# Performance work log

Measured on AMD Instinct MI355X. Metric: run time of the kernel, lower is better.

The kernel has to match this reference:

```python
import jax, jax.numpy as jnp
import numpy as np

N_EMBD = 384
N_HEAD = 6
HEAD_SIZE = N_EMBD // N_HEAD
D_FF = 4 * N_EMBD
LN_EPS = 1e-3  # keras LayerNormalization default epsilon


def setup_inputs() -> dict:
    key = jax.random.key(0)
    ks = jax.random.split(key, 12)
    B, T = 4, 2048
    s = 1.0 / np.sqrt(N_EMBD)
    return {
        "x": jax.random.normal(ks[0], (B, T, N_EMBD), dtype=jnp.float32),
        "Wq": jax.random.normal(ks[1], (N_EMBD, N_EMBD), dtype=jnp.float32) * s,
        "Wk": jax.random.normal(ks[2], (N_EMBD, N_EMBD), dtype=jnp.float32) * s,
        "Wv": jax.random.normal(ks[3], (N_EMBD, N_EMBD), dtype=jnp.float32) * s,
        "Wo": jax.random.normal(ks[4], (N_EMBD, N_EMBD), dtype=jnp.float32) * s,
        "bo": jnp.zeros((N_EMBD,), dtype=jnp.float32),
        "W1": jax.random.normal(ks[5], (N_EMBD, D_FF), dtype=jnp.float32) * s,
        "b1": jnp.zeros((D_FF,), dtype=jnp.float32),
        "W2": jax.random.normal(ks[6], (D_FF, N_EMBD), dtype=jnp.float32) * (1.0 / np.sqrt(D_FF)),
        "b2": jnp.zeros((N_EMBD,), dtype=jnp.float32),
        "g1": jnp.ones((N_EMBD,), dtype=jnp.float32),
        "be1": jnp.zeros((N_EMBD,), dtype=jnp.float32),
        "g2": jnp.ones((N_EMBD,), dtype=jnp.float32),
        "be2": jnp.zeros((N_EMBD,), dtype=jnp.float32),
    }


def _layer_norm(x, gamma, beta):
    mu = jnp.mean(x, axis=-1, keepdims=True)
    var = jnp.mean(jnp.square(x - mu), axis=-1, keepdims=True)
    return (x - mu) * jax.lax.rsqrt(var + LN_EPS) * gamma + beta


def _block(x, Wq, Wk, Wv, Wo, bo, W1, b1, W2, b2, g1, be1, g2, be2):
    B, T, C = x.shape
    H, D = N_HEAD, HEAD_SIZE
    q = (x @ Wq).reshape(B, T, H, D).transpose(0, 2, 1, 3)  # [B,H,T,D]
    k = (x @ Wk).reshape(B, T, H, D).transpose(0, 2, 1, 3)
    v = (x @ Wv).reshape(B, T, H, D).transpose(0, 2, 1, 3)
    scores = jnp.einsum("bhqd,bhkd->bhqk", q, k) / jnp.sqrt(jnp.float32(D))
    causal = jnp.tril(jnp.ones((T, T), dtype=bool))
    scores = jnp.where(causal, scores, jnp.float32(-1e9))
    attn = jax.nn.softmax(scores, axis=-1)  # dropout is identity at inference
    out = jnp.einsum("bhqk,bhkd->bhqd", attn, v)
    out = out.transpose(0, 2, 1, 3).reshape(B, T, H * D)
    y = out @ Wo + bo
    x = _layer_norm(x + y, g1, be1)
    y = jax.nn.relu(x @ W1 + b1) @ W2 + b2
    return _layer_norm(x + y, g2, be2)


def reference(x, Wq, Wk, Wv, Wo, bo, W1, b1, W2, b2, g1, be1, g2, be2):
    return _block(x, Wq, Wk, Wv, Wo, bo, W1, b1, W2, b2, g1, be1, g2, be2)
```

## Files before the change

kernel.cpp:

```cpp
#include <hip/hip_runtime.h>

#define C_DIM  384
#define HEADS  6
#define HD     64
#define FF_DIM 1536
#define LN_EPS 1e-3f
#define TSEQ   2048
#define BATCH  4
#define LOG2E  1.4426950408889634f
#define QK_SCALE 0.18033688011112042f

typedef __attribute__((ext_vector_type(4))) float          f32x4;
typedef __attribute__((ext_vector_type(4))) float          float4_t;
typedef __attribute__((ext_vector_type(8))) short          bfrag;
typedef __attribute__((ext_vector_type(4))) unsigned short ushort4_t;
typedef __attribute__((ext_vector_type(8))) unsigned short ushort8_t;

__device__ inline unsigned short f2bf(float f) {
    unsigned int u = __builtin_bit_cast(unsigned int, f);
    u += 0x7fff + ((u >> 16) & 1);
    return (unsigned short)(u >> 16);
}
__device__ inline unsigned short f2bf_t(float f) {
    return (unsigned short)(__builtin_bit_cast(unsigned int, f) >> 16);
}

__device__ inline void gload_lds16(const void* g, void* l) {
    __builtin_amdgcn_global_load_lds(
        (const __attribute__((address_space(1))) unsigned int*)g,
        (__attribute__((address_space(3))) unsigned int*)l,
        16, 0, 0);
}

__global__ __launch_bounds__(256)
void transpose_w4(const float* __restrict__ Wq, const float* __restrict__ Wk,
                  const float* __restrict__ Wv, const float* __restrict__ Wo,
                  unsigned short* __restrict__ Dq, unsigned short* __restrict__ Dk,
                  unsigned short* __restrict__ Dv, unsigned short* __restrict__ Do_)
{
    __shared__ float tile[32][33];
    const int z = blockIdx.z;
    const float* W = z == 0 ? Wq : (z == 1 ? Wk : (z == 2 ? Wv : Wo));
    unsigned short* D = z == 0 ? Dq : (z == 1 ? Dk : (z == 2 ? Dv : Do_));
    const int tx = threadIdx.x, ty = threadIdx.y;
    const int n0 = blockIdx.x * 32, k0 = blockIdx.y * 32;
    #pragma unroll
    for (int i = 0; i < 32; i += 8)
        tile[ty + i][tx] = W[(size_t)(k0 + ty + i) * C_DIM + n0 + tx];
    __syncthreads();
    #pragma unroll
    for (int i = 0; i < 32; i += 8)
        D[(size_t)(n0 + ty + i) * C_DIM + k0 + tx] = f2bf(tile[tx][ty + i]);
}

__global__ __launch_bounds__(256)
void transpose_w(const float* __restrict__ W, unsigned short* __restrict__ Wt, int K, int N)
{
    __shared__ float tile[32][33];
    const int tx = threadIdx.x, ty = threadIdx.y;
    const int n0 = blockIdx.x * 32, k0 = blockIdx.y * 32;
    #pragma unroll
    for (int i = 0; i < 32; i += 8)
        tile[ty + i][tx] = W[(size_t)(k0 + ty + i) * N + n0 + tx];
    __syncthreads();
    #pragma unroll
    for (int i = 0; i < 32; i += 8)
        Wt[(size_t)(n0 + ty + i) * K + k0 + tx] = f2bf(tile[tx][ty + i]);
}

__global__ __launch_bounds__(256)
void cvt_f32_bf16_x4(const float* __restrict__ in, unsigned short* __restrict__ out, int n4)
{
    int i = blockIdx.x * 256 + threadIdx.x;
    if (i >= n4) return;
    float4_t v = ((const float4_t*)in)[i];
    ushort4_t o = { f2bf(v.x), f2bf(v.y), f2bf(v.z), f2bf(v.w) };
    ((ushort4_t*)out)[i] = o;
}

__global__ __launch_bounds__(256)
void vtrans_kernel(const unsigned short* __restrict__ qkv,
                   unsigned short* __restrict__ vt,
                   unsigned short* __restrict__ ktc)
{
    __shared__ unsigned short tile[32][34];
    const int tx = threadIdx.x, ty = threadIdx.y;
    const int bh = blockIdx.z, b = bh / HEADS, h = bh % HEADS;
    const int t0 = blockIdx.x * 32, d0 = blockIdx.y * 32;
    #pragma unroll
    for (int i = 0; i < 32; i += 8) {
        tile[ty + i][tx] = qkv[(size_t)(b * TSEQ + t0 + ty + i) * 1152 + 2 * C_DIM + h * HD + d0 + tx];
        ktc[((size_t)bh * TSEQ + t0 + ty + i) * HD + d0 + tx] =
            qkv[(size_t)(b * TSEQ + t0 + ty + i) * 1152 + C_DIM + h * HD + d0 + tx];
    }
    __syncthreads();
    #pragma unroll
    for (int i = 0; i < 32; i += 8)
        vt[((size_t)bh * HD + d0 + ty + i) * TSEQ + t0 + tx] = tile[tx][ty + i];
}

template<int OBF16, int BIAS, int RELU, int QSCALE>
__global__ __launch_bounds__(256)
void gemm_lds(const unsigned short* __restrict__ A, const unsigned short* __restrict__ Bt,
              const float* __restrict__ bias, void* __restrict__ Cv,
              int M, int N, int K)
{
    __shared__ __align__(16) unsigned short As[16 * 512];
    __shared__ __align__(16) unsigned short Bs[16 * 512];

    const int t = threadIdx.x, lane = t & 63, w = t >> 6;
    const int ln16 = lane & 15, hi16 = lane >> 4;
    const int wr = w >> 1, wc = w & 1;
    const int row0 = blockIdx.y * 128, col0 = blockIdx.x * 128;

    f32x4 acc[4][4] = {};

    for (int k0 = 0; k0 < K; k0 += 64) {
        #pragma unroll
        for (int i = 0; i < 4; ++i) {
            const int f  = w * 4 + i;
            const int ks = f >> 3, rf = f & 7;
            const int row = rf * 16 + ln16;
            const int kc  = k0 + ks * 32 + hi16 * 8;
            gload_lds16(&A [(size_t)(row0 + row) * K + kc], &As[f * 512]);
            gload_lds16(&Bt[(size_t)(col0 + row) * K + kc], &Bs[f * 512]);
        }
        __syncthreads();
        #pragma unroll
        for (int ks = 0; ks < 2; ++ks) {
            bfrag a[4], b[4];
            #pragma unroll
            for (int i = 0; i < 4; ++i)
                a[i] = *(const bfrag*)&As[(ks * 8 + wr * 4 + i) * 512 + lane * 8];
            #pragma unroll
            for (int j = 0; j < 4; ++j)
                b[j] = *(const bfrag*)&Bs[(ks * 8 + wc * 4 + j) * 512 + lane * 8];
            #pragma unroll
            for (int i = 0; i < 4; ++i)
                #pragma unroll
                for (int j = 0; j < 4; ++j)
                    acc[i][j] = __builtin_amdgcn_mfma_f32_16x16x32_bf16(a[i], b[j], acc[i][j], 0, 0, 0);
        }
        __syncthreads();
    }

    #pragma unroll
    for (int j = 0; j < 4; ++j) {
        const int col = col0 + wc * 64 + j * 16 + ln16;
        const float bv = BIAS ? bias[col] : 0.0f;
        const float sc = (QSCALE && col < C_DIM) ? QK_SCALE : 1.0f;
        #pragma unroll
        for (int i = 0; i < 4; ++i) {
            #pragma unroll
            for (int e = 0; e < 4; ++e) {
                const int row = row0 + wr * 64 + i * 16 + hi16 * 4 + e;
                float v = acc[i][j][e] + bv;
                if (RELU) v = fmaxf(v, 0.0f);
                if (QSCALE) v *= sc;
                if (OBF16) ((unsigned short*)Cv)[(size_t)row * N + col] = f2bf(v);
                else       ((float*)Cv)[(size_t)row * N + col] = v;
            }
        }
    }
}

template<int OBF16, int BIAS, int RELU>
__global__ __launch_bounds__(256)
void gemm_lds64(const unsigned short* __restrict__ A, const unsigned short* __restrict__ Bt,
                const float* __restrict__ bias, void* __restrict__ Cv,
                int M, int N, int K)
{
    __shared__ __align__(16) unsigned short As[8 * 512];
    __shared__ __align__(16) unsigned short Bs[16 * 512];

    const int t = threadIdx.x, lane = t & 63, w = t >> 6;
    const int ln16 = lane & 15, hi16 = lane >> 4;
    const int wr = w >> 1, wc = w & 1;
    const int row0 = blockIdx.y * 64, col0 = blockIdx.x * 128;

    f32x4 acc[2][4] = {};

    for (int k0 = 0; k0 < K; k0 += 64) {
        #pragma unroll
        for (int i = 0; i < 2; ++i) {
            const int f  = w * 2 + i;
            const int ks = f >> 2, rf = f & 3;
            gload_lds16(&A[(size_t)(row0 + rf * 16 + ln16) * K + k0 + ks * 32 + hi16 * 8],
                        &As[f * 512]);
        }
        #pragma unroll
        for (int i = 0; i < 4; ++i) {
            const int f  = w * 4 + i;
            const int ks = f >> 3, cf = f & 7;
            gload_lds16(&Bt[(size_t)(col0 + cf * 16 + ln16) * K + k0 + ks * 32 + hi16 * 8],
                        &Bs[f * 512]);
        }
        __syncthreads();
        #pragma unroll
        for (int ks = 0; ks < 2; ++ks) {
            bfrag a[2], b[4];
            #pragma unroll
            for (int i = 0; i < 2; ++i)
                a[i] = *(const bfrag*)&As[(ks * 4 + wr * 2 + i) * 512 + lane * 8];
            #pragma unroll
            for (int j = 0; j < 4; ++j)
                b[j] = *(const bfrag*)&Bs[(ks * 8 + wc * 4 + j) * 512 + lane * 8];
            #pragma unroll
            for (int i = 0; i < 2; ++i)
                #pragma unroll
                for (int j = 0; j < 4; ++j)
                    acc[i][j] = __builtin_amdgcn_mfma_f32_16x16x32_bf16(a[i], b[j], acc[i][j], 0, 0, 0);
        }
        __syncthreads();
    }

    #pragma unroll
    for (int j = 0; j < 4; ++j) {
        const int col = col0 + wc * 64 + j * 16 + ln16;
        const float bv = BIAS ? bias[col] : 0.0f;
        #pragma unroll
        for (int i = 0; i < 2; ++i) {
            #pragma unroll
            for (int e = 0; e < 4; ++e) {
                const int row = row0 + wr * 32 + i * 16 + hi16 * 4 + e;
                float v = acc[i][j][e] + bv;
                if (RELU) v = fmaxf(v, 0.0f);
                if (OBF16) ((unsigned short*)Cv)[(size_t)row * N + col] = f2bf(v);
                else       ((float*)Cv)[(size_t)row * N + col] = v;
            }
        }
    }
}

__device__ inline void qk16(const bfrag (&qf)[2][2], const bfrag (&kf)[4][2],
                            f32x4 (&sf)[2][4])
{
    #pragma unroll
    for (int jt = 0; jt < 4; ++jt)
        #pragma unroll
        for (int ks = 0; ks < 2; ++ks) {
            sf[0][jt] = __builtin_amdgcn_mfma_f32_16x16x32_bf16(qf[0][ks], kf[jt][ks], sf[0][jt], 0, 0, 0);
            sf[1][jt] = __builtin_amdgcn_mfma_f32_16x16x32_bf16(qf[1][ks], kf[jt][ks], sf[1][jt], 0, 0, 0);
        }
}

__device__ inline void softmax_pv(f32x4 (&sf)[2][4], const bfrag (&vf)[4][2],
                                  f32x4 (&acc)[2][4],
                                  float (&mrow)[2][4], float (&lrow)[2][4],
                                  unsigned short (*Ps)[72],
                                  int tok0, int kt, bool last, int ln16, int hi16)
{
    float lmax[2][4];
    bool need = false;
    #pragma unroll
    for (int rf = 0; rf < 2; ++rf)
        #pragma unroll
        for (int e = 0; e < 4; ++e) {
            const int row = tok0 + rf * 16 + hi16 * 4 + e;
            float mx = -1e30f;
            #pragma unroll
            for (int jt = 0; jt < 4; ++jt) {
                float sv = sf[rf][jt][e];
                if (last && (kt * 64 + jt * 16 + ln16 > row)) sv = -1e30f;
                mx = fmaxf(mx, sv);
            }
            lmax[rf][e] = mx;
            need = need || (mx > mrow[rf][e] + 8.0f);
        }
    if (__any(need)) {
        #pragma unroll
        for (int rf = 0; rf < 2; ++rf)
            #pragma unroll
            for (int e = 0; e < 4; ++e) {
                float rm = lmax[rf][e];
                rm = fmaxf(rm, __shfl_xor(rm, 1));
                rm = fmaxf(rm, __shfl_xor(rm, 2));
                rm = fmaxf(rm, __shfl_xor(rm, 4));
                rm = fmaxf(rm, __shfl_xor(rm, 8));
                const float mn = fmaxf(mrow[rf][e], rm);
                const float corr = exp2f(mrow[rf][e] - mn);
                mrow[rf][e] = mn;
                lrow[rf][e] *= corr;
                #pragma unroll
                for (int dt = 0; dt < 4; ++dt) acc[rf][dt][e] *= corr;
            }
    }

    #pragma unroll
    for (int rf = 0; rf < 2; ++rf)
        #pragma unroll
        for (int jt = 0; jt < 4; ++jt)
            #pragma unroll
            for (int e = 0; e < 4; ++e) {
                const int row = tok0 + rf * 16 + hi16 * 4 + e;
                float sv = sf[rf][jt][e];
                if (last && (kt * 64 + jt * 16 + ln16 > row)) sv = -1e30f;
                const float pe = exp2f(sv - mrow[rf][e]);
                lrow[rf][e] += pe;
                Ps[rf * 16 + hi16 * 4 + e][jt * 16 + ln16] = f2bf_t(pe);
            }

    bfrag pf[2][2];
    #pragma unroll
    for (int rf = 0; rf < 2; ++rf)
        #pragma unroll
        for (int ks = 0; ks < 2; ++ks)
            pf[rf][ks] = *(const bfrag*)&Ps[rf * 16 + ln16][ks * 32 + hi16 * 8];
    #pragma unroll
    for (int ks = 0; ks < 2; ++ks)
        #pragma unroll
        for (int rf = 0; rf < 2; ++rf)
            #pragma unroll
            for (int dt = 0; dt < 4; ++dt)
                acc[rf][dt] = __builtin_amdgcn_mfma_f32_16x16x32_bf16(pf[rf][ks], vf[dt][ks], acc[rf][dt], 0, 0, 0);
}

__global__ __launch_bounds__(128)
void attn_kernel(const unsigned short* __restrict__ qkv,
                 const unsigned short* __restrict__ ktc,
                 const unsigned short* __restrict__ vt,
                 unsigned short* __restrict__ att)
{
    __shared__ __align__(16) unsigned short Klds[2][4096];
    __shared__ __align__(16) unsigned short Vlds[2][4096];
    __shared__ __align__(16) unsigned short Ps[2][32][72];

    const int tid  = threadIdx.x;
    const int lane = tid & 63, wid = tid >> 6;
    const int ln16 = lane & 15, hi16 = lane >> 4;
    const int bid = blockIdx.x;
    const int xcd = bid & 7;
    const int i2  = bid >> 3;
    const int j   = i2 / 3;
    const int bh  = xcd * 3 + (i2 % 3);
    const int qw  = 63 - (j * 2 + wid);
    const int b   = bh / HEADS, h = bh % HEADS;
    const int tok0 = qw * 32;
    const size_t qrow0 = (size_t)b * TSEQ;
    const int NT = 32 - j;

    bfrag qf[2][2];
    #pragma unroll
    for (int rf = 0; rf < 2; ++rf)
        #pragma unroll
        for (int ks = 0; ks < 2; ++ks)
            qf[rf][ks] = *(const bfrag*)&qkv[(qrow0 + tok0 + rf * 16 + ln16) * 1152 + h * HD + ks * 32 + hi16 * 8];

    f32x4 acc[2][4] = {};
    float mrow[2][4], lrow[2][4];
    #pragma unroll
    for (int rf = 0; rf < 2; ++rf)
        #pragma unroll
        for (int e = 0; e < 4; ++e) { mrow[rf][e] = -1e30f; lrow[rf][e] = 0.0f; }

    const unsigned short* Kb = ktc + (size_t)bh * TSEQ * HD;
    const unsigned short* Vb = vt  + (size_t)bh * HD * TSEQ;

    int off[4][2];
    #pragma unroll
    for (int jt = 0; jt < 4; ++jt)
        #pragma unroll
        for (int ks = 0; ks < 2; ++ks) {
            const int row = jt * 16 + ln16;
            off[jt][ks] = row * 128 + ((ks * 64 + hi16 * 16) ^ ((row & 7) << 4));
        }

    auto stage = [&](int bf, int kt) {
        #pragma unroll
        for (int i = 0; i < 4; ++i) {
            const int g   = wid * 4 + i;
            const int c16 = g * 64 + lane;
            const int r   = c16 >> 3;
            const int s16 = (c16 & 7) ^ (r & 7);
            gload_lds16(&Kb[(size_t)(kt * 64 + r) * HD + s16 * 8], &Klds[bf][g * 512]);
            gload_lds16(&Vb[(size_t)r * TSEQ + kt * 64 + s16 * 8], &Vlds[bf][g * 512]);
        }
    };

    int buf = 0;
    stage(0, 0);
    __syncthreads();

    for (int kt = 0; kt < NT; ++kt) {
        if (kt + 1 < NT) stage(buf ^ 1, kt + 1);

        const char* Kb8 = (const char*)&Klds[buf][0];
        const char* Vb8 = (const char*)&Vlds[buf][0];
        bfrag kf[4][2], vf[4][2];
        #pragma unroll
        for (int jt = 0; jt < 4; ++jt)
            #pragma unroll
            for (int ks = 0; ks < 2; ++ks) {
                kf[jt][ks] = *(const bfrag*)(Kb8 + off[jt][ks]);
                vf[jt][ks] = *(const bfrag*)(Vb8 + off[jt][ks]);
            }

        f32x4 sf[2][4] = {};
        qk16(qf, kf, sf);
        softmax_pv(sf, vf, acc, mrow, lrow, Ps[wid], tok0, kt, kt == NT - 1, ln16, hi16);

        __syncthreads();
        buf ^= 1;
    }

    #pragma unroll
    for (int rf = 0; rf < 2; ++rf)
        #pragma unroll
        for (int e = 0; e < 4; ++e) {
            float l = lrow[rf][e];
            l += __shfl_xor(l, 1);
            l += __shfl_xor(l, 2);
            l += __shfl_xor(l, 4);
            l += __shfl_xor(l, 8);
            const float inv = 1.0f / l;
            const size_t row = qrow0 + tok0 + rf * 16 + hi16 * 4 + e;
            #pragma unroll
            for (int dt = 0; dt < 4; ++dt)
                att[row * C_DIM + h * HD + dt * 16 + ln16] = f2bf(acc[rf][dt][e] * inv);
        }
}

template<int WB>
__global__ __launch_bounds__(256)
void ln_residual_kernel(const float* __restrict__ A, const float* __restrict__ R,
                        const float* __restrict__ gamma, const float* __restrict__ beta,
                        float* __restrict__ out, unsigned short* __restrict__ outb, int Mrows)
{
    const int lane = threadIdx.x & 63;
    const int wv   = threadIdx.x >> 6;
    const int row  = blockIdx.x * 4 + wv;
    if (row >= Mrows) return;
    const size_t off = (size_t)row * C_DIM;

    float v[6];
    float sum = 0.0f;
    #pragma unroll
    for (int j = 0; j < 6; ++j) {
        const int c = lane + 64 * j;
        v[j] = A[off + c] + R[off + c];
        sum += v[j];
    }
    #pragma unroll
    for (int o = 1; o < 64; o <<= 1) sum += __shfl_xor(sum, o);
    const float mu = sum * (1.0f / C_DIM);

    float sq = 0.0f;
    #pragma unroll
    for (int j = 0; j < 6; ++j) { const float d = v[j] - mu; sq = fmaf(d, d, sq); }
    #pragma unroll
    for (int o = 1; o < 64; o <<= 1) sq += __shfl_xor(sq, o);
    const float rstd = rsqrtf(sq * (1.0f / C_DIM) + LN_EPS);

    #pragma unroll
    for (int j = 0; j < 6; ++j) {
        const int c = lane + 64 * j;
        const float r = (v[j] - mu) * rstd * gamma[c] + beta[c];
        out[off + c] = r;
        if (WB) outb[off + c] = f2bf(r);
    }
}

extern "C" void kernel_launch(void* const* d_in, const int* in_sizes, int n_in,
                              void* d_out, int out_size, void* d_ws, size_t ws_size,
                              hipStream_t stream)
{
    const float* x   = (const float*)d_in[0];
    const float* Wq  = (const float*)d_in[1];
    const float* Wk  = (const float*)d_in[2];
    const float* Wv  = (const float*)d_in[3];
    const float* Wo  = (const float*)d_in[4];
    const float* bo  = (const float*)d_in[5];
    const float* W1  = (const float*)d_in[6];
    const float* b1  = (const float*)d_in[7];
    const float* W2  = (const float*)d_in[8];
    const float* b2  = (const float*)d_in[9];
    const float* g1  = (const float*)d_in[10];
    const float* be1 = (const float*)d_in[11];
    const float* g2  = (const float*)d_in[12];
    const float* be2 = (const float*)d_in[13];
    float* out = (float*)d_out;

    const int M = BATCH * TSEQ;
    const size_t MC = (size_t)M * C_DIM;

    char* ws = (char*)d_ws;
    unsigned short* qkv = (unsigned short*)ws;
    unsigned short* vt  = (unsigned short*)(ws + (size_t)M*1152*2);
    unsigned short* att = (unsigned short*)(ws + (size_t)M*1152*2 + (size_t)BATCH*HEADS*HD*TSEQ*2);
    unsigned short* h1  = (unsigned short*)ws;
    char* p2 = ws + (size_t)M*1152*2 + (size_t)BATCH*HEADS*HD*TSEQ*2 + MC*2;
    unsigned short* xb  = (unsigned short*)p2;
    unsigned short* ktc = xb;
    float* y   = (float*)(p2 + MC*2);
    float* x1  = (float*)(p2 + MC*2 + MC*4);
    unsigned short* x1b = (unsigned short*)(p2 + MC*2 + 2*MC*4);
    char* p3 = p2 + MC*2 + 2*MC*4 + MC*2;
    unsigned short* Wqkv_t = (unsigned short*)p3;
    unsigned short* Wo_t   = Wqkv_t + (size_t)3*C_DIM*C_DIM;
    unsigned short* W1_t   = Wo_t   + (size_t)C_DIM*C_DIM;
    unsigned short* W2_t   = W1_t   + (size_t)FF_DIM*C_DIM;

    dim3 b256(256), b328(32, 8);

    transpose_w4<<<dim3(C_DIM/32, C_DIM/32, 4), b328, 0, stream>>>(
        Wq, Wk, Wv, Wo,
        Wqkv_t, Wqkv_t + (size_t)C_DIM*C_DIM, Wqkv_t + (size_t)2*C_DIM*C_DIM, Wo_t);
    transpose_w<<<dim3(FF_DIM/32, C_DIM/32), b328, 0, stream>>>(W1, W1_t, C_DIM, FF_DIM);
    transpose_w<<<dim3(C_DIM/32, FF_DIM/32), b328, 0, stream>>>(W2, W2_t, FF_DIM, C_DIM);

    cvt_f32_bf16_x4<<<dim3((MC/4 + 255)/256), b256, 0, stream>>>(x, xb, (int)(MC/4));

    gemm_lds<1, 0, 0, 1><<<dim3(3*C_DIM/128, M/128), b256, 0, stream>>>(
        xb, Wqkv_t, nullptr, qkv, M, 3*C_DIM, C_DIM);

    vtrans_kernel<<<dim3(TSEQ/32, HD/32, BATCH*HEADS), b328, 0, stream>>>(qkv, vt, ktc);

    attn_kernel<<<dim3(768), dim3(128), 0, stream>>>(qkv, ktc, vt, att);

    gemm_lds64<0, 1, 0><<<dim3(C_DIM/128, M/64), b256, 0, stream>>>(
        att, Wo_t, bo, y, M, C_DIM, C_DIM);

    ln_residual_kernel<1><<<dim3(M/4), b256, 0, stream>>>(x, y, g1, be1, x1, x1b, M);

    gemm_lds<1, 1, 1, 0><<<dim3(FF_DIM/128, M/128), b256, 0, stream>>>(
        x1b, W1_t, b1, h1, M, FF_DIM, C_DIM);

    gemm_lds64<0, 1, 0><<<dim3(C_DIM/128, M/64), b256, 0, stream>>>(
        h1, W2_t, b2, y, M, C_DIM, FF_DIM);

    ln_residual_kernel<0><<<dim3(M/4), b256, 0, stream>>>(x1, y, g2, be2, out, nullptr, M);
}
```

Before: 211.0 us.

## Split heavy causal attention rows across two KV chunks with a combine kernel

The attention kernel becomes single-wave blocks. The 32 heaviest query tiles per head are split into two KV halves, each written as unnormalized bf16 partial outputs with row max and sum, and a new combine kernel merges them. The LDS double-buffered K/V staging and block syncs are replaced by direct global register loads with K prefetched one tile ahead. This aims to balance the causal workload across more blocks, at the cost of an extra launch, partial-result traffic, and bf16 rounding of the partials.

```diff
diff --git a/kernel.cpp b/kernel.cpp
--- a/kernel.cpp
+++ b/kernel.cpp
@@ -315,29 +315,44 @@
                 acc[rf][dt] = __builtin_amdgcn_mfma_f32_16x16x32_bf16(pf[rf][ks], vf[dt][ks], acc[rf][dt], 0, 0, 0);
 }
 
-__global__ __launch_bounds__(128)
+__global__ __launch_bounds__(64)
 void attn_kernel(const unsigned short* __restrict__ qkv,
                  const unsigned short* __restrict__ ktc,
                  const unsigned short* __restrict__ vt,
-                 unsigned short* __restrict__ att)
-{
-    __shared__ __align__(16) unsigned short Klds[2][4096];
-    __shared__ __align__(16) unsigned short Vlds[2][4096];
-    __shared__ __align__(16) unsigned short Ps[2][32][72];
-
-    const int tid  = threadIdx.x;
-    const int lane = tid & 63, wid = tid >> 6;
+                 unsigned short* __restrict__ att,
+                 unsigned short* __restrict__ pacc,
+                 float* __restrict__ pml)
+{
+    __shared__ __align__(16) unsigned short Ps[32][72];
+    const int lane = threadIdx.x;
     const int ln16 = lane & 15, hi16 = lane >> 4;
     const int bid = blockIdx.x;
     const int xcd = bid & 7;
-    const int i2  = bid >> 3;
-    const int j   = i2 / 3;
-    const int bh  = xcd * 3 + (i2 % 3);
-    const int qw  = 63 - (j * 2 + wid);
-    const int b   = bh / HEADS, h = bh % HEADS;
+    const int i   = bid >> 3;
+    int bh, qw, kt0, kte, ck = 0;
+    bool heavy;
+    if (i < 192) {
+        qw = 63 - (i / 6);
+        const int r = i % 6;
+        bh = xcd * 3 + (r >> 1);
+        ck = r & 1;
+        const int NT = (qw >> 1) + 1;
+        const int half = NT >> 1;
+        kt0 = ck ? half : 0;
+        kte = ck ? NT : half;
+        heavy = true;
+    } else {
+        const int j = i - 192;
+        qw = 31 - (j / 3);
+        bh = xcd * 3 + (j % 3);
+        kt0 = 0;
+        kte = (qw >> 1) + 1;
+        heavy = false;
+    }
+    const int NTfull = (qw >> 1) + 1;
+    const int b = bh / HEADS, h = bh % HEADS;
     const int tok0 = qw * 32;
     const size_t qrow0 = (size_t)b * TSEQ;
-    const int NT = 32 - j;
 
     bfrag qf[2][2];
     #pragma unroll
@@ -356,53 +371,36 @@
     const unsigned short* Kb = ktc + (size_t)bh * TSEQ * HD;
     const unsigned short* Vb = vt  + (size_t)bh * HD * TSEQ;
 
-    int off[4][2];
+    bfrag kf[4][2];
     #pragma unroll
     for (int jt = 0; jt < 4; ++jt)
         #pragma unroll
-        for (int ks = 0; ks < 2; ++ks) {
-            const int row = jt * 16 + ln16;
-            off[jt][ks] = row * 128 + ((ks * 64 + hi16 * 16) ^ ((row & 7) << 4));
-        }
-
-    auto stage = [&](int bf, int kt) {
-        #pragma unroll
-        for (int i = 0; i < 4; ++i) {
-            const int g   = wid * 4 + i;
-            const int c16 = g * 64 + lane;
-            const int r   = c16 >> 3;
-            const int s16 = (c16 & 7) ^ (r & 7);
-            gload_lds16(&Kb[(size_t)(kt * 64 + r) * HD + s16 * 8], &Klds[bf][g * 512]);
-            gload_lds16(&Vb[(size_t)r * TSEQ + kt * 64 + s16 * 8], &Vlds[bf][g * 512]);
-        }
-    };
-
-    int buf = 0;
-    stage(0, 0);
-    __syncthreads();
-
-    for (int kt = 0; kt < NT; ++kt) {
-        if (kt + 1 < NT) stage(buf ^ 1, kt + 1);
-
-        const char* Kb8 = (const char*)&Klds[buf][0];
-        const char* Vb8 = (const char*)&Vlds[buf][0];
-        bfrag kf[4][2], vf[4][2];
-        #pragma unroll
-        for (int jt = 0; jt < 4; ++jt)
-            #pragma unroll
-            for (int ks = 0; ks < 2; ++ks) {
-                kf[jt][ks] = *(const bfrag*)(Kb8 + off[jt][ks]);
-                vf[jt][ks] = *(const bfrag*)(Vb8 + off[jt][ks]);
-            }
+        for (int ks = 0; ks < 2; ++ks)
+            kf[jt][ks] = *(const bfrag*)&Kb[(size_t)(kt0 * 64 + jt * 16 + ln16) * HD + ks * 32 + hi16 * 8];
+
+    for (int kt = kt0; kt < kte; ++kt) {
+        bfrag vf[4][2];
+        #pragma unroll
+        for (int dt = 0; dt < 4; ++dt)
+            #pragma unroll
+            for (int ks = 0; ks < 2; ++ks)
+                vf[dt][ks] = *(const bfrag*)&Vb[(size_t)(dt * 16 + ln16) * TSEQ + kt * 64 + ks * 32 + hi16 * 8];
 
         f32x4 sf[2][4] = {};
         qk16(qf, kf, sf);
-        softmax_pv(sf, vf, acc, mrow, lrow, Ps[wid], tok0, kt, kt == NT - 1, ln16, hi16);
-
-        __syncthreads();
-        buf ^= 1;
-    }
-
+
+        if (kt + 1 < kte) {
+            #pragma unroll
+            for (int jt = 0; jt < 4; ++jt)
+                #pragma unroll
+                for (int ks = 0; ks < 2; ++ks)
+                    kf[jt][ks] = *(const bfrag*)&Kb[(size_t)((kt + 1) * 64 + jt * 16 + ln16) * HD + ks * 32 + hi16 * 8];
+        }
+
+        softmax_pv(sf, vf, acc, mrow, lrow, Ps, tok0, kt, kt == NTfull - 1, ln16, hi16);
+    }
+
+    float lsum[2][4];
     #pragma unroll
     for (int rf = 0; rf < 2; ++rf)
         #pragma unroll
@@ -412,12 +410,77 @@
             l += __shfl_xor(l, 2);
             l += __shfl_xor(l, 4);
             l += __shfl_xor(l, 8);
-            const float inv = 1.0f / l;
-            const size_t row = qrow0 + tok0 + rf * 16 + hi16 * 4 + e;
+            lsum[rf][e] = l;
+        }
+
+    if (!heavy) {
+        #pragma unroll
+        for (int rf = 0; rf < 2; ++rf)
+            #pragma unroll
+            for (int e = 0; e < 4; ++e) {
+                const float inv = 1.0f / lsum[rf][e];
+                const size_t row = qrow0 + tok0 + rf * 16 + hi16 * 4 + e;
+                #pragma unroll
+                for (int dt = 0; dt < 4; ++dt)
+                    att[row * C_DIM + h * HD + dt * 16 + ln16] = f2bf(acc[rf][dt][e] * inv);
+            }
+    } else {
+        const int sidx = bh * 32 + (qw - 32);
+        const size_t pb = (size_t)sidx * 2 + ck;
+        #pragma unroll
+        for (int rf = 0; rf < 2; ++rf)
             #pragma unroll
             for (int dt = 0; dt < 4; ++dt)
-                att[row * C_DIM + h * HD + dt * 16 + ln16] = f2bf(acc[rf][dt][e] * inv);
-        }
+                #pragma unroll
+                for (int e = 0; e < 4; ++e) {
+                    const int row = rf * 16 + hi16 * 4 + e;
+                    pacc[(pb * 32 + row) * 64 + dt * 16 + ln16] = f2bf(acc[rf][dt][e]);
+                }
+        if (ln16 == 0) {
+            #pragma unroll
+            for (int rf = 0; rf < 2; ++rf)
+                #pragma unroll
+                for (int e = 0; e < 4; ++e) {
+                    const int row = rf * 16 + hi16 * 4 + e;
+                    pml[pb * 64 + row * 2 + 0] = mrow[rf][e];
+                    pml[pb * 64 + row * 2 + 1] = lsum[rf][e];
+                }
+        }
+    }
+}
+
+__global__ __launch_bounds__(256)
+void attn_combine(const unsigned short* __restrict__ pacc,
+                  const float* __restrict__ pml,
+                  unsigned short* __restrict__ att)
+{
+    const int sidx = blockIdx.x;
+    const int bh = sidx >> 5;
+    const int qw = 32 + (sidx & 31);
+    const int b = bh / HEADS, h = bh % HEADS;
+    const int tid = threadIdx.x;
+    const int row = tid >> 3;
+    const int d0  = (tid & 7) * 8;
+
+    const float m0 = pml[((size_t)sidx * 2 + 0) * 64 + row * 2 + 0];
+    const float l0 = pml[((size_t)sidx * 2 + 0) * 64 + row * 2 + 1];
+    const float m1 = pml[((size_t)sidx * 2 + 1) * 64 + row * 2 + 0];
+    const float l1 = pml[((size_t)sidx * 2 + 1) * 64 + row * 2 + 1];
+    const float M  = fmaxf(m0, m1);
+    const float w0 = exp2f(m0 - M), w1 = exp2f(m1 - M);
+    const float invL = 1.0f / (l0 * w0 + l1 * w1);
+
+    ushort8_t a0 = *(const ushort8_t*)&pacc[(((size_t)sidx * 2 + 0) * 32 + row) * 64 + d0];
+    ushort8_t a1 = *(const ushort8_t*)&pacc[(((size_t)sidx * 2 + 1) * 32 + row) * 64 + d0];
+    ushort8_t rv;
+    #pragma unroll
+    for (int k = 0; k < 8; ++k) {
+        const float v0 = __builtin_bit_cast(float, (unsigned int)a0[k] << 16);
+        const float v1 = __builtin_bit_cast(float, (unsigned int)a1[k] << 16);
+        rv[k] = f2bf((v0 * w0 + v1 * w1) * invL);
+    }
+    const size_t grow = (size_t)b * TSEQ + qw * 32 + row;
+    *(ushort8_t*)&att[grow * C_DIM + h * HD + d0] = rv;
 }
 
 template<int WB>
@@ -500,6 +563,9 @@
     unsigned short* W1_t   = Wo_t   + (size_t)C_DIM*C_DIM;
     unsigned short* W2_t   = W1_t   + (size_t)FF_DIM*C_DIM;
 
+    unsigned short* pacc = (unsigned short*)(p2 + MC*2);
+    float* pml = (float*)(p2 + MC*2 + (size_t)1536*32*64*2);
+
     dim3 b256(256), b328(32, 8);
 
     transpose_w4<<<dim3(C_DIM/32, C_DIM/32, 4), b328, 0, stream>>>(
@@ -515,7 +581,8 @@
 
     vtrans_kernel<<<dim3(TSEQ/32, HD/32, BATCH*HEADS), b328, 0, stream>>>(qkv, vt, ktc);
 
-    attn_kernel<<<dim3(768), dim3(128), 0, stream>>>(qkv, ktc, vt, att);
+    attn_kernel<<<dim3(2304), dim3(64), 0, stream>>>(qkv, ktc, vt, att, pacc, pml);
+    attn_combine<<<dim3(768), b256, 0, stream>>>(pacc, pml, att);
 
     gemm_lds64<0, 1, 0><<<dim3(C_DIM/128, M/64), b256, 0, stream>>>(
         att, Wo_t, bo, y, M, C_DIM, C_DIM);
```

Result: faster. 204.1 us (-3.3%).
